# Kernel tuning notes

Hardware: AMD Instinct MI355X
Metric: run time of the kernel (lower is better)

The kernel has to match this reference:

```python
import jax, jax.numpy as jnp
import numpy as np
import math

N = 50000          # number of nodes
K = 32             # fixed neighbor-list degree
D_IN = 256
D_OUT = 256
TPERC = 0.45


def setup_inputs() -> dict:
    key = jax.random.key(0)
    k1, k2, k3 = jax.random.split(key, 3)
    x = jax.random.normal(k1, (N, D_IN), dtype=jnp.float32)
    nbrs = jax.random.randint(k2, (N, K), 0, N, dtype=jnp.int64)
    # nn.Linear weight: [out_features, in_features], scaled ~1/sqrt(fan_in)
    W = jax.random.normal(k3, (D_OUT, D_IN), dtype=jnp.float32) / np.sqrt(D_IN)
    return {"x": x, "nbrs": nbrs, "W": W}


def reference(x, nbrs, W):
    # h = Linear(x): [N, D_OUT]
    h = jnp.einsum("ni,oi->no", x, W)
    # gather neighbor messages: [N, K, D_OUT]
    msgs = h[nbrs]
    # per-node sort over the neighbor axis (feature-wise, as torch.sort(dim=0))
    msgs = jnp.sort(msgs, axis=1)
    remove = math.floor(K * TPERC)  # static trim count (14 when K=32)
    if remove > 0:
        msgs = msgs[:, remove:K - remove]
    # trimmed mean over remaining neighbors: [N, D_OUT]
    return jnp.mean(msgs, axis=1)
```

## Files before the change

### kernel.cpp

```cpp
#include <hip/hip_runtime.h>
#include <hip/hip_fp16.h>

#define D      256
#define NNODES 50000
#define KNBR   32
#define NGRP   8
#define GRPC   32

typedef _Float16 h8 __attribute__((ext_vector_type(8)));
typedef _Float16 h4 __attribute__((ext_vector_type(4)));
typedef _Float16 h2 __attribute__((ext_vector_type(2)));
typedef float    f4 __attribute__((ext_vector_type(4)));

__device__ __forceinline__ h2 h2min(h2 a, h2 b) {
  h2 d; asm("v_pk_min_f16 %0, %1, %2" : "=v"(d) : "v"(a), "v"(b)); return d;
}
__device__ __forceinline__ h2 h2max(h2 a, h2 b) {
  h2 d; asm("v_pk_max_f16 %0, %1, %2" : "=v"(d) : "v"(a), "v"(b)); return d;
}

__device__ __forceinline__ void gll16(const void* g, void* l) {
  __builtin_amdgcn_global_load_lds(
      (const __attribute__((address_space(1))) void*)g,
      (__attribute__((address_space(3))) void*)l, 16, 0, 0);
}


__global__ void wcvt(const float* __restrict__ W, _Float16* __restrict__ whi) {
  int i = (blockIdx.x * 256 + threadIdx.x) * 4;
  float4 w = *(const float4*)&W[i];
  union { _Float16 h[4]; uint2 u; } H;
  H.h[0] = (_Float16)w.x; H.h[1] = (_Float16)w.y;
  H.h[2] = (_Float16)w.z; H.h[3] = (_Float16)w.w;
  *(uint2*)&whi[i] = H.u;
}

__global__ __launch_bounds__(256, 4)
void gemm_mfma(const float* __restrict__ x, const _Float16* __restrict__ Whi,
               _Float16* __restrict__ hblk) {
  __shared__ _Float16 Ws[2][4][128][8];

  const int tid  = threadIdx.x;
  const int lane = tid & 63;
  const int wv   = tid >> 6;
  const int wvu  = __builtin_amdgcn_readfirstlane(wv);
  const int c    = lane & 15;
  const int ko   = lane >> 4;
  const int brow = blockIdx.x * 128;
  const int bcol = blockIdx.y * 128;

  const float* xrow[2];
#pragma unroll
  for (int tl = 0; tl < 2; tl++) {
    int ar = brow + wv * 32 + tl * 16 + c;
    if (ar >= NNODES) ar = NNODES - 1;
    xrow[tl] = &x[(size_t)ar * D];
  }

  f4 acc[2][8];
#pragma unroll
  for (int tl = 0; tl < 2; tl++)
#pragma unroll
    for (int j = 0; j < 8; j++) acc[tl][j] = (f4)(0.f);

  auto stage = [&](int buf, int t) {
    const int k0 = t * 32;
#pragma unroll
    for (int q = 0; q < 2; q++) {
      const int fb   = wvu * 128 + q * 64;
      const int f    = fb + lane;
      const int kq   = f >> 7;
      const int colL = f & 127;
      gll16(&Whi[(size_t)(bcol + colL) * D + k0 + kq * 8],
            (char*)Ws + ((size_t)buf * 512 + fb) * 16);
    }
  };

  stage(0, 0);
  __syncthreads();

  float4 xa[2][2], xb[2][2];
#pragma unroll
  for (int tl = 0; tl < 2; tl++) {
    xa[tl][0] = *(const float4*)(xrow[tl] + ko * 8);
    xa[tl][1] = *(const float4*)(xrow[tl] + ko * 8 + 4);
  }

  for (int t = 0; t < 8; ++t) {
    const int buf = t & 1;
    if (t < 7) {
      stage(buf ^ 1, t + 1);
#pragma unroll
      for (int tl = 0; tl < 2; tl++) {
        xb[tl][0] = *(const float4*)(xrow[tl] + (t + 1) * 32 + ko * 8);
        xb[tl][1] = *(const float4*)(xrow[tl] + (t + 1) * 32 + ko * 8 + 4);
      }
    }

    h8 ahi[2], alo[2];
#pragma unroll
    for (int tl = 0; tl < 2; tl++) {
      float xf[8] = {xa[tl][0].x, xa[tl][0].y, xa[tl][0].z, xa[tl][0].w,
                     xa[tl][1].x, xa[tl][1].y, xa[tl][1].z, xa[tl][1].w};
#pragma unroll
      for (int e = 0; e < 8; e++) {
        _Float16 hi = (_Float16)xf[e];
        ahi[tl][e] = hi;
        alo[tl][e] = (_Float16)(xf[e] - (float)hi);
      }
    }

#pragma unroll
    for (int j = 0; j < 8; j++) {
      h8 bhi = *(const h8*)&Ws[buf][ko][j * 16 + c][0];
#pragma unroll
      for (int tl = 0; tl < 2; tl++) {
        acc[tl][j] = __builtin_amdgcn_mfma_f32_16x16x32_f16(ahi[tl], bhi, acc[tl][j], 0, 0, 0);
        acc[tl][j] = __builtin_amdgcn_mfma_f32_16x16x32_f16(alo[tl], bhi, acc[tl][j], 0, 0, 0);
      }
    }

    if (t < 7) {
      __syncthreads();
#pragma unroll
      for (int tl = 0; tl < 2; tl++) { xa[tl][0] = xb[tl][0]; xa[tl][1] = xb[tl][1]; }
    }
  }

#pragma unroll
  for (int tl = 0; tl < 2; tl++)
#pragma unroll
    for (int j = 0; j < 8; j++) {
      const int g  = (bcol >> 5) + (j >> 1);
      const int oc = (j & 1) * 16 + c;
#pragma unroll
      for (int r = 0; r < 4; r++) {
        const int n = brow + wv * 32 + tl * 16 + ko * 4 + r;
        if (n < NNODES)
          hblk[((size_t)g * NNODES + n) * GRPC + oc] = (_Float16)acc[tl][j][r];
      }
    }
}

template <int N, int P, int K>
__device__ __forceinline__ void oem_pass(h2* v) {
#pragma unroll
  for (int j = K % P; j + K < N; j += 2 * K) {
#pragma unroll
    for (int i = 0; i < K; i++) {
      if (i + j + K < N && ((i + j) / (2 * P) == (i + j + K) / (2 * P))) {
        h2 lo = h2min(v[i + j], v[i + j + K]);
        h2 hi = h2max(v[i + j], v[i + j + K]);
        v[i + j] = lo;
        v[i + j + K] = hi;
      }
    }
  }
}

__device__ __forceinline__ void sort16(h2* v) {
  oem_pass<16, 1, 1>(v);
  oem_pass<16, 2, 2>(v);  oem_pass<16, 2, 1>(v);
  oem_pass<16, 4, 4>(v);  oem_pass<16, 4, 2>(v);  oem_pass<16, 4, 1>(v);
  oem_pass<16, 8, 8>(v);  oem_pass<16, 8, 4>(v);  oem_pass<16, 8, 2>(v);
  oem_pass<16, 8, 1>(v);
}

__device__ __forceinline__ void ce(h2* v, int a, int b) {
  h2 lo = h2min(v[a], v[b]);
  h2 hi = h2max(v[a], v[b]);
  v[a] = lo; v[b] = hi;
}

__device__ __forceinline__ void select_mid4(h2* v) {
  sort16(v);
  sort16(v + 16);
#pragma unroll
  for (int i = 0; i < 16; i++) ce(v, i, 31 - i);
#pragma unroll
  for (int i = 0; i < 8; i++) ce(v, i, i + 8);
#pragma unroll
  for (int i = 8; i < 12; i++) ce(v, i, i + 4);
  ce(v, 12, 14); ce(v, 13, 15);
#pragma unroll
  for (int i = 16; i < 24; i++) ce(v, i, i + 8);
#pragma unroll
  for (int i = 16; i < 20; i++) ce(v, i, i + 4);
  ce(v, 16, 18); ce(v, 17, 19);
}

__global__ __launch_bounds__(256, 4)
void trimmed_gather(const _Float16* __restrict__ hblk, const int* __restrict__ nbrs,
                    float* __restrict__ out) {
  __shared__ int nb[32 * KNBR];
  const int bid   = blockIdx.x;
  const int g     = bid & 7;
  const int chunk = bid >> 3;
  const int n0    = chunk * 32;
  const int t     = threadIdx.x;

#pragma unroll
  for (int q = 0; q < 4; q++) {
    int idx = n0 * KNBR + q * 256 + t;
    if (idx >= NNODES * KNBR) idx = NNODES * KNBR - 1;
    nb[q * 256 + t] = nbrs[idx];
  }
  __syncthreads();

  const int nl = t >> 3;
  const int cp = t & 7;
  const _Float16* base = hblk + (size_t)g * NNODES * GRPC + cp * 4;

  h2 va[KNBR], vb[KNBR];
#pragma unroll
  for (int k = 0; k < KNBR; k++) {
    const int r = nb[nl * KNBR + k];
    h4 w = *(const h4*)(base + (size_t)r * GRPC);
    va[k] = __builtin_shufflevector(w, w, 0, 1);
    vb[k] = __builtin_shufflevector(w, w, 2, 3);
  }

  select_mid4(va);
  select_mid4(vb);

  float4 res;
  res.x = ((float)va[14][0] + (float)va[15][0] + (float)va[16][0] + (float)va[17][0]) * 0.25f;
  res.y = ((float)va[14][1] + (float)va[15][1] + (float)va[16][1] + (float)va[17][1]) * 0.25f;
  res.z = ((float)vb[14][0] + (float)vb[15][0] + (float)vb[16][0] + (float)vb[17][0]) * 0.25f;
  res.w = ((float)vb[14][1] + (float)vb[15][1] + (float)vb[16][1] + (float)vb[17][1]) * 0.25f;

  const int n = n0 + nl;
  if (n < NNODES)
    *(float4*)&out[(size_t)n * D + g * GRPC + cp * 4] = res;
}

extern "C" void kernel_launch(void* const* d_in, const int* in_sizes, int n_in,
                              void* d_out, int out_size, void* d_ws, size_t ws_size,
                              hipStream_t stream) {
  const float* x    = (const float*)d_in[0];
  const int*   nbrs = (const int*)d_in[1];
  const float* W    = (const float*)d_in[2];
  float*       out  = (float*)d_out;

  _Float16* hblk = (_Float16*)d_ws;
  _Float16* Whi  = (_Float16*)((char*)d_ws + 25600000);

  wcvt<<<dim3(64), dim3(256), 0, stream>>>(W, Whi);
  gemm_mfma<<<dim3((NNODES + 127) / 128, 2), dim3(256), 0, stream>>>(x, Whi, hblk);
  trimmed_gather<<<dim3(NGRP * ((NNODES + 31) / 32)), dim3(256), 0, stream>>>(
      hblk, nbrs, out);
}
```

Baseline: 205.4 us.

## Fully unroll GEMM k-loop with explicit waitcnt barriers and tune gather kernel

The GEMM k-loop is fully unrolled and keeps every x tile in its own register slot. The __syncthreads at the end of each step becomes a partial s_waitcnt vmcnt(4) plus s_barrier, with sched_barriers so the prefetch loads can stay in flight during the MFMAs. GEMM occupancy is lowered to 2 blocks per SM to give more registers, and the gather kernel is raised to 8. The neighbor-index LDS array is padded to stride 33 to avoid bank conflicts, and packed f16 min/max switch from inline asm to builtins the compiler can schedule. The risks are register pressure from the unrolled x buffers, and correctness if vmcnt(4) does not match the actual number of outstanding loads.

```diff
diff --git a/kernel.cpp b/kernel.cpp
--- a/kernel.cpp
+++ b/kernel.cpp
@@ -11,13 +11,6 @@
 typedef _Float16 h4 __attribute__((ext_vector_type(4)));
 typedef _Float16 h2 __attribute__((ext_vector_type(2)));
 typedef float    f4 __attribute__((ext_vector_type(4)));
-
-__device__ __forceinline__ h2 h2min(h2 a, h2 b) {
-  h2 d; asm("v_pk_min_f16 %0, %1, %2" : "=v"(d) : "v"(a), "v"(b)); return d;
-}
-__device__ __forceinline__ h2 h2max(h2 a, h2 b) {
-  h2 d; asm("v_pk_max_f16 %0, %1, %2" : "=v"(d) : "v"(a), "v"(b)); return d;
-}
 
 __device__ __forceinline__ void gll16(const void* g, void* l) {
   __builtin_amdgcn_global_load_lds(
@@ -35,7 +28,7 @@
   *(uint2*)&whi[i] = H.u;
 }
 
-__global__ __launch_bounds__(256, 4)
+__global__ __launch_bounds__(256, 2)
 void gemm_mfma(const float* __restrict__ x, const _Float16* __restrict__ Whi,
                _Float16* __restrict__ hblk) {
   __shared__ _Float16 Ws[2][4][128][8];
@@ -76,32 +69,35 @@
     }
   };
 
+  float4 xv[8][2][2];
+
   stage(0, 0);
+#pragma unroll
+  for (int tl = 0; tl < 2; tl++) {
+    xv[0][tl][0] = *(const float4*)(xrow[tl] + ko * 8);
+    xv[0][tl][1] = *(const float4*)(xrow[tl] + ko * 8 + 4);
+  }
   __syncthreads();
 
-  float4 xa[2][2], xb[2][2];
-#pragma unroll
-  for (int tl = 0; tl < 2; tl++) {
-    xa[tl][0] = *(const float4*)(xrow[tl] + ko * 8);
-    xa[tl][1] = *(const float4*)(xrow[tl] + ko * 8 + 4);
-  }
-
+#pragma unroll
   for (int t = 0; t < 8; ++t) {
     const int buf = t & 1;
     if (t < 7) {
       stage(buf ^ 1, t + 1);
+      __builtin_amdgcn_sched_barrier(0);
 #pragma unroll
       for (int tl = 0; tl < 2; tl++) {
-        xb[tl][0] = *(const float4*)(xrow[tl] + (t + 1) * 32 + ko * 8);
-        xb[tl][1] = *(const float4*)(xrow[tl] + (t + 1) * 32 + ko * 8 + 4);
-      }
+        xv[t + 1][tl][0] = *(const float4*)(xrow[tl] + (t + 1) * 32 + ko * 8);
+        xv[t + 1][tl][1] = *(const float4*)(xrow[tl] + (t + 1) * 32 + ko * 8 + 4);
+      }
+      __builtin_amdgcn_sched_barrier(0);
     }
 
     h8 ahi[2], alo[2];
 #pragma unroll
     for (int tl = 0; tl < 2; tl++) {
-      float xf[8] = {xa[tl][0].x, xa[tl][0].y, xa[tl][0].z, xa[tl][0].w,
-                     xa[tl][1].x, xa[tl][1].y, xa[tl][1].z, xa[tl][1].w};
+      float xf[8] = {xv[t][tl][0].x, xv[t][tl][0].y, xv[t][tl][0].z, xv[t][tl][0].w,
+                     xv[t][tl][1].x, xv[t][tl][1].y, xv[t][tl][1].z, xv[t][tl][1].w};
 #pragma unroll
       for (int e = 0; e < 8; e++) {
         _Float16 hi = (_Float16)xf[e];
@@ -121,9 +117,9 @@
     }
 
     if (t < 7) {
-      __syncthreads();
-#pragma unroll
-      for (int tl = 0; tl < 2; tl++) { xa[tl][0] = xb[tl][0]; xa[tl][1] = xb[tl][1]; }
+      asm volatile("s_waitcnt vmcnt(4)" ::: "memory");
+      __builtin_amdgcn_s_barrier();
+      __builtin_amdgcn_sched_barrier(0);
     }
   }
 
@@ -140,6 +136,13 @@
           hblk[((size_t)g * NNODES + n) * GRPC + oc] = (_Float16)acc[tl][j][r];
       }
     }
+}
+
+__device__ __forceinline__ h2 h2min(h2 a, h2 b) {
+  return __builtin_elementwise_min(a, b);
+}
+__device__ __forceinline__ h2 h2max(h2 a, h2 b) {
+  return __builtin_elementwise_max(a, b);
 }
 
 template <int N, int P, int K>
@@ -189,10 +192,10 @@
   ce(v, 16, 18); ce(v, 17, 19);
 }
 
-__global__ __launch_bounds__(256, 4)
+__global__ __launch_bounds__(256, 8)
 void trimmed_gather(const _Float16* __restrict__ hblk, const int* __restrict__ nbrs,
                     float* __restrict__ out) {
-  __shared__ int nb[32 * KNBR];
+  __shared__ int nb[32 * 33];
   const int bid   = blockIdx.x;
   const int g     = bid & 7;
   const int chunk = bid >> 3;
@@ -201,9 +204,10 @@
 
 #pragma unroll
   for (int q = 0; q < 4; q++) {
-    int idx = n0 * KNBR + q * 256 + t;
+    int e   = q * 256 + t;
+    int idx = n0 * KNBR + e;
     if (idx >= NNODES * KNBR) idx = NNODES * KNBR - 1;
-    nb[q * 256 + t] = nbrs[idx];
+    nb[(e >> 5) * 33 + (e & 31)] = nbrs[idx];
   }
   __syncthreads();
 
@@ -214,7 +218,7 @@
   h2 va[KNBR], vb[KNBR];
 #pragma unroll
   for (int k = 0; k < KNBR; k++) {
-    const int r = nb[nl * KNBR + k];
+    const int r = nb[nl * 33 + k];
     h4 w = *(const h4*)(base + (size_t)r * GRPC);
     va[k] = __builtin_shufflevector(w, w, 0, 1);
     vb[k] = __builtin_shufflevector(w, w, 2, 3);
```

Measured after the change: 609.4 us. +196.7%, slower.
